# Kernel tuning notes

Hardware: AMD Instinct MI355X
Metric: run time of the kernel (lower is better)

## Reference

```python
import jax, jax.numpy as jnp
import numpy as np

B, N, T, F, D = 2, 8, 128, 128, 256
EPS = 1e-5


def setup_inputs() -> dict:
    key = jax.random.key(0)
    ks = jax.random.split(key, 8)
    s = 1.0 / np.sqrt(D)
    s2 = 1.0 / np.sqrt(2 * D)
    return {
        "x": jax.random.normal(ks[0], (B, N, D), dtype=jnp.float32),
        "t_emb": jax.random.normal(ks[1], (T, D), dtype=jnp.float32),
        "f_emb": jax.random.normal(ks[2], (F, D), dtype=jnp.float32),
        "ln_g": jnp.ones((D,), dtype=jnp.float32),
        "ln_b": jnp.zeros((D,), dtype=jnp.float32),
        "W1": jax.random.uniform(ks[3], (D, 2 * D), jnp.float32, -s, s),
        "b1": jax.random.uniform(ks[4], (2 * D,), jnp.float32, -s, s),
        "W2": jax.random.uniform(ks[5], (2 * D, 2), jnp.float32, -s2, s2),
        "b2": jax.random.uniform(ks[6], (2,), jnp.float32, -s2, s2),
    }


def reference(x, t_emb, f_emb, ln_g, ln_b, W1, b1, W2, b2):
    # x: [B,N,D]; pos_emb: [T,F,D]; broadcast-add -> [B,N,T,F,D]
    pos = t_emb[:, None, :] + f_emb[None, :, :]            # [T,F,D]
    h = x[:, :, None, None, :] + pos[None, None]           # [B,N,T,F,D]
    # LayerNorm over last dim
    mu = jnp.mean(h, axis=-1, keepdims=True)
    var = jnp.mean(jnp.square(h - mu), axis=-1, keepdims=True)
    h = (h - mu) * jax.lax.rsqrt(var + EPS) * ln_g + ln_b
    # MLP: D -> 2D -> 2
    h = jax.nn.relu(jnp.einsum("bntfd,de->bntfe", h, W1) + b1)
    out = jnp.einsum("bntfe,eo->bntfo", h, W2) + b2        # [B,N,T,F,2]
    return out
```

## Files before the change

### kernel.cpp

```cpp
#include <hip/hip_runtime.h>
#include <stdint.h>


#define D_ 256
#define E_ 512

typedef __attribute__((ext_vector_type(8))) short short8;
typedef __attribute__((ext_vector_type(4))) short short4v;
typedef __attribute__((ext_vector_type(4))) float f32x4;
typedef __attribute__((ext_vector_type(2))) float f32x2;

__device__ alignas(16) unsigned short g_Abuf[2176 * 768];
__device__ alignas(16) unsigned short g_Bbuf[768 * 640];
__device__ alignas(16) float g_U[2048 * 512];
__device__ alignas(16) float g_C[2048 * 128];
__device__ alignas(16) float g_Vt[512 * 128];
__device__ alignas(16) float g_GKW[512 * 4];
__device__ alignas(16) float g_sxt[2048];
__device__ alignas(16) float g_sqxt[2048];
__device__ alignas(16) float g_sf[128];
__device__ alignas(16) float g_sqf[128];

__device__ inline unsigned short f2bf(float f) {
  unsigned int u = __float_as_uint(f);
  u += 0x7fffu + ((u >> 16) & 1u);
  return (unsigned short)(u >> 16);
}
__device__ inline float bf2f(unsigned short h) {
  return __uint_as_float(((unsigned int)h) << 16);
}

__global__ __launch_bounds__(256) void prep(
    const float* __restrict__ x, const float* __restrict__ t_emb,
    const float* __restrict__ f_emb, const float* __restrict__ ln_g,
    const float* __restrict__ ln_b, const float* __restrict__ W1,
    const float* __restrict__ b1, const float* __restrict__ W2) {
  const int blk = blockIdx.x;
  const int tid = threadIdx.x;
  if (blk < 544) {
    const int l = tid & 63;
    int arow;
    float v0, v1, v2, v3;
    if (blk < 512) {
      const int r = blk * 4 + (tid >> 6);
      const int bn = r >> 7, t = r & 127;
      const float4 xv = *(const float4*)(x + bn * D_ + 4 * l);
      const float4 tv = *(const float4*)(t_emb + t * D_ + 4 * l);
      v0 = xv.x + tv.x; v1 = xv.y + tv.y;
      v2 = xv.z + tv.z; v3 = xv.w + tv.w;
      arow = r;
    } else {
      const int fi = (blk - 512) * 4 + (tid >> 6);
      const float4 fv = *(const float4*)(f_emb + fi * D_ + 4 * l);
      v0 = fv.x; v1 = fv.y; v2 = fv.z; v3 = fv.w;
      arow = 2048 + fi;
    }
    union { unsigned short u[4]; short4v v; } hi, lo;
    hi.u[0] = f2bf(v0); hi.u[1] = f2bf(v1);
    hi.u[2] = f2bf(v2); hi.u[3] = f2bf(v3);
    lo.u[0] = f2bf(v0 - bf2f(hi.u[0]));
    lo.u[1] = f2bf(v1 - bf2f(hi.u[1]));
    lo.u[2] = f2bf(v2 - bf2f(hi.u[2]));
    lo.u[3] = f2bf(v3 - bf2f(hi.u[3]));
    unsigned short* ab = g_Abuf + arow * 768 + 4 * l;
    *(short4v*)(ab) = hi.v;
    *(short4v*)(ab + 256) = lo.v;
    *(short4v*)(ab + 512) = hi.v;
    float s = (v0 + v1) + (v2 + v3);
    float q = fmaf(v0, v0, fmaf(v1, v1, fmaf(v2, v2, v3 * v3)));
#pragma unroll
    for (int d = 1; d < 64; d <<= 1) {
      s += __shfl_xor(s, d);
      q += __shfl_xor(q, d);
    }
    if (l == 0) {
      if (blk < 512) { g_sxt[arow] = s; g_sqxt[arow] = q; }
      else           { g_sf[arow - 2048] = s; g_sqf[arow - 2048] = q; }
    }
  } else if (blk < 552) {
    __shared__ float red[4][64][2];
    const int w = tid >> 6, l = tid & 63;
    const int e = (blk - 544) * 64 + l;
    const int k0 = w * 64;
    float G = 0.f, K = 0.f;
#pragma unroll 8
    for (int i = 0; i < 64; ++i) {
      const float wv = W1[(k0 + i) * E_ + e];
      G = fmaf(ln_g[k0 + i], wv, G);
      K = fmaf(ln_b[k0 + i], wv, K);
    }
    red[w][l][0] = G;
    red[w][l][1] = K;
    __syncthreads();
    if (w == 0) {
      G = (red[0][l][0] + red[1][l][0]) + (red[2][l][0] + red[3][l][0]);
      K = (red[0][l][1] + red[1][l][1]) + (red[2][l][1] + red[3][l][1]);
      float4 o;
      o.x = G; o.y = K + b1[e];
      o.z = W2[2 * e]; o.w = W2[2 * e + 1];
      *(float4*)(g_GKW + 4 * e) = o;
    }
  } else {
    const int gidx = (blk - 552) * 256 + tid;
    const int lane = gidx & 63;
    const int jtl = (gidx >> 6) & 3;
    const int cc = gidx >> 8;
    const int ct = cc % 10;
    const int kt = cc / 10;
    const int col = ct * 64 + jtl * 16 + (lane & 15);
    const int kbase = kt * 32 + ((lane >> 4) & 3) * 8;
    union { unsigned short u[8]; short8 v; } fr;
#pragma unroll
    for (int j = 0; j < 8; ++j) {
      const int kk = kbase + j;
      const int term = kk >> 8;
      const int k = kk & 255;
      float v;
      if (col < 512) v = ln_g[k] * W1[k * E_ + col];
      else           v = f_emb[(col - 512) * D_ + k];
      const unsigned short h = f2bf(v);
      fr.u[j] = (term == 2) ? f2bf(v - bf2f(h)) : h;
    }
    *(short8*)(g_Bbuf + gidx * 8) = fr.v;
  }
}

__global__ __launch_bounds__(256) void gemm3() {
  const int tid = threadIdx.x;
  const int wave = tid >> 6, lane = tid & 63;
  const int quad = (lane >> 4) & 3, n16 = lane & 15;
  const int rt = blockIdx.x / 10, ct = blockIdx.x % 10;
  const int rowb = rt * 128 + wave * 32;

  const unsigned short* a0 = g_Abuf + (size_t)(rowb + n16) * 768 + quad * 8;
  const unsigned short* a1 = a0 + 16 * 768;

  f32x4 acc[2][4];
#pragma unroll
  for (int j = 0; j < 4; ++j) {
    acc[0][j] = (f32x4){0.f, 0.f, 0.f, 0.f};
    acc[1][j] = (f32x4){0.f, 0.f, 0.f, 0.f};
  }

#pragma unroll 4
  for (int kt = 0; kt < 24; ++kt) {
    const short8 av0 = *(const short8*)(a0 + kt * 32);
    const short8 av1 = *(const short8*)(a1 + kt * 32);
    const short8* bp = (const short8*)g_Bbuf + ((kt * 10 + ct) * 4) * 64 + lane;
#pragma unroll
    for (int jtl = 0; jtl < 4; ++jtl) {
      const short8 bf = bp[jtl * 64];
      acc[0][jtl] =
          __builtin_amdgcn_mfma_f32_16x16x32_bf16(av0, bf, acc[0][jtl], 0, 0, 0);
      acc[1][jtl] =
          __builtin_amdgcn_mfma_f32_16x16x32_bf16(av1, bf, acc[1][jtl], 0, 0, 0);
    }
  }

#pragma unroll
  for (int g = 0; g < 2; ++g)
#pragma unroll
    for (int jtl = 0; jtl < 4; ++jtl)
#pragma unroll
      for (int r = 0; r < 4; ++r) {
        const float val = acc[g][jtl][r];
        const int grow = rowb + g * 16 + quad * 4 + r;
        const int col = ct * 64 + jtl * 16 + n16;
        if (rt < 16) {
          if (ct < 8) g_U[grow * 512 + col] = val;
          else        g_C[grow * 128 + (col - 512)] = val;
        } else if (ct < 8) {
          g_Vt[col * 128 + (grow - 2048)] = val;
        }
      }
}

__global__ __launch_bounds__(512) void decode2(const float* __restrict__ b2,
                                               float* __restrict__ out) {
  __shared__ float part[8][64][17];
  const int tid = threadIdx.x;
  const int w = tid >> 6, lane = tid & 63;
  const int bnt0 = blockIdx.x * 4;

  const f32x2 sf2 = *(const f32x2*)(g_sf + 2 * lane);
  const f32x2 sqf2 = *(const f32x2*)(g_sqf + 2 * lane);
  f32x2 Ar[4], Br[4];
#pragma unroll
  for (int ti = 0; ti < 4; ++ti) {
    const float sx = g_sxt[bnt0 + ti];
    const float sqx = g_sqxt[bnt0 + ti];
    const f32x2 c2 = *(const f32x2*)(g_C + (bnt0 + ti) * 128 + 2 * lane);
    const f32x2 mu = (sf2 + sx) * (1.0f / 256.0f);
    const f32x2 var = (sqf2 + 2.0f * c2 + sqx) * (1.0f / 256.0f) - mu * mu;
    f32x2 rs;
    rs.x = rsqrtf(var.x + 1e-5f);
    rs.y = rsqrtf(var.y + 1e-5f);
    Ar[ti] = rs;
    Br[ti] = -rs * mu;
  }

  f32x2 o0[4] = {(f32x2){0.f, 0.f}, (f32x2){0.f, 0.f},
                 (f32x2){0.f, 0.f}, (f32x2){0.f, 0.f}};
  f32x2 o1[4] = {(f32x2){0.f, 0.f}, (f32x2){0.f, 0.f},
                 (f32x2){0.f, 0.f}, (f32x2){0.f, 0.f}};
  const int ebase = __builtin_amdgcn_readfirstlane(w * 64);
#pragma unroll 8
  for (int ei = 0; ei < 64; ++ei) {
    const int e = ebase + ei;
    const float4 gkw = *(const float4*)(g_GKW + 4 * e);
    const f32x2 v2 = *(const f32x2*)(g_Vt + e * 128 + 2 * lane);
#pragma unroll
    for (int ti = 0; ti < 4; ++ti) {
      const float u = g_U[(bnt0 + ti) * 512 + e];
      const f32x2 s = v2 + u;
      const f32x2 pre = Ar[ti] * s + (Br[ti] * gkw.x + gkw.y);
      f32x2 y;
      y.x = fmaxf(pre.x, 0.f);
      y.y = fmaxf(pre.y, 0.f);
      o0[ti] += y * gkw.z;
      o1[ti] += y * gkw.w;
    }
  }

#pragma unroll
  for (int ti = 0; ti < 4; ++ti) {
    part[w][lane][ti * 4 + 0] = o0[ti].x;
    part[w][lane][ti * 4 + 1] = o1[ti].x;
    part[w][lane][ti * 4 + 2] = o0[ti].y;
    part[w][lane][ti * 4 + 3] = o1[ti].y;
  }
  __syncthreads();

  const int t = tid >> 7, f = tid & 127;
  const int m = f >> 1, ff = f & 1;
  float r0 = b2[0], r1 = b2[1];
#pragma unroll
  for (int w2 = 0; w2 < 8; ++w2) {
    r0 += part[w2][m][t * 4 + ff * 2 + 0];
    r1 += part[w2][m][t * 4 + ff * 2 + 1];
  }
  float2 res;
  res.x = r0;
  res.y = r1;
  *(float2*)(out + ((bnt0 + t) * 128 + f) * 2) = res;
}

extern "C" void kernel_launch(void* const* d_in, const int* in_sizes, int n_in,
                              void* d_out, int out_size, void* d_ws,
                              size_t ws_size, hipStream_t stream) {
  const float* x = (const float*)d_in[0];
  const float* t_emb = (const float*)d_in[1];
  const float* f_emb = (const float*)d_in[2];
  const float* ln_g = (const float*)d_in[3];
  const float* ln_b = (const float*)d_in[4];
  const float* W1 = (const float*)d_in[5];
  const float* b1 = (const float*)d_in[6];
  const float* W2 = (const float*)d_in[7];
  const float* b2 = (const float*)d_in[8];
  (void)d_ws; (void)ws_size;

  prep<<<792, 256, 0, stream>>>(x, t_emb, f_emb, ln_g, ln_b, W1, b1, W2);
  gemm3<<<170, 256, 0, stream>>>();
  decode2<<<512, 512, 0, stream>>>(b2, (float*)d_out);
}
```

Baseline: 113.2 us.

## Fuse prep, GEMM and decode into one persistent kernel with grid barriers

Merges the three kernels into a single 512-block launch whose phases are separated by a software grid barrier built on an atomic counter. This removes two launch gaps and inter-kernel drains. Work is redistributed per wave: the GEMM now uses one 16-row tile per wave, and the decode uses 256-thread blocks with 128 e values per wave. The barrier assumes all 512 blocks are co-resident, and the spin-wait plus reduced per-wave reuse in the GEMM may add cost.

```diff
diff --git a/kernel.cpp b/kernel.cpp
--- a/kernel.cpp
+++ b/kernel.cpp
@@ -4,6 +4,7 @@
 
 #define D_ 256
 #define E_ 512
+#define NBLK 512
 
 typedef __attribute__((ext_vector_type(8))) short short8;
 typedef __attribute__((ext_vector_type(4))) short short4v;
@@ -20,6 +21,7 @@
 __device__ alignas(16) float g_sqxt[2048];
 __device__ alignas(16) float g_sf[128];
 __device__ alignas(16) float g_sqf[128];
+__device__ unsigned int g_bar = 0;
 
 __device__ inline unsigned short f2bf(float f) {
   unsigned int u = __float_as_uint(f);
@@ -30,219 +32,218 @@
   return __uint_as_float(((unsigned int)h) << 16);
 }
 
-__global__ __launch_bounds__(256) void prep(
+__device__ inline void grid_barrier() {
+  __syncthreads();
+  if (threadIdx.x == 0) {
+    __threadfence();
+    const unsigned old =
+        __hip_atomic_fetch_add(&g_bar, 1u, __ATOMIC_RELAXED,
+                               __HIP_MEMORY_SCOPE_AGENT);
+    const unsigned target = (old & ~(unsigned)(NBLK - 1)) + NBLK;
+    while (__hip_atomic_load(&g_bar, __ATOMIC_RELAXED,
+                             __HIP_MEMORY_SCOPE_AGENT) < target)
+      __builtin_amdgcn_s_sleep(2);
+    __threadfence();
+  }
+  __syncthreads();
+}
+
+__global__ __launch_bounds__(256, 2) void fused(
     const float* __restrict__ x, const float* __restrict__ t_emb,
     const float* __restrict__ f_emb, const float* __restrict__ ln_g,
     const float* __restrict__ ln_b, const float* __restrict__ W1,
-    const float* __restrict__ b1, const float* __restrict__ W2) {
+    const float* __restrict__ b1, const float* __restrict__ W2,
+    const float* __restrict__ b2, float* __restrict__ out) {
+  __shared__ float part[4][64][17];
+  const int tid = threadIdx.x;
   const int blk = blockIdx.x;
-  const int tid = threadIdx.x;
-  if (blk < 544) {
-    const int l = tid & 63;
-    int arow;
-    float v0, v1, v2, v3;
-    if (blk < 512) {
-      const int r = blk * 4 + (tid >> 6);
-      const int bn = r >> 7, t = r & 127;
-      const float4 xv = *(const float4*)(x + bn * D_ + 4 * l);
-      const float4 tv = *(const float4*)(t_emb + t * D_ + 4 * l);
-      v0 = xv.x + tv.x; v1 = xv.y + tv.y;
-      v2 = xv.z + tv.z; v3 = xv.w + tv.w;
-      arow = r;
-    } else {
-      const int fi = (blk - 512) * 4 + (tid >> 6);
-      const float4 fv = *(const float4*)(f_emb + fi * D_ + 4 * l);
-      v0 = fv.x; v1 = fv.y; v2 = fv.z; v3 = fv.w;
-      arow = 2048 + fi;
-    }
-    union { unsigned short u[4]; short4v v; } hi, lo;
-    hi.u[0] = f2bf(v0); hi.u[1] = f2bf(v1);
-    hi.u[2] = f2bf(v2); hi.u[3] = f2bf(v3);
-    lo.u[0] = f2bf(v0 - bf2f(hi.u[0]));
-    lo.u[1] = f2bf(v1 - bf2f(hi.u[1]));
-    lo.u[2] = f2bf(v2 - bf2f(hi.u[2]));
-    lo.u[3] = f2bf(v3 - bf2f(hi.u[3]));
-    unsigned short* ab = g_Abuf + arow * 768 + 4 * l;
-    *(short4v*)(ab) = hi.v;
-    *(short4v*)(ab + 256) = lo.v;
-    *(short4v*)(ab + 512) = hi.v;
-    float s = (v0 + v1) + (v2 + v3);
-    float q = fmaf(v0, v0, fmaf(v1, v1, fmaf(v2, v2, v3 * v3)));
-#pragma unroll
-    for (int d = 1; d < 64; d <<= 1) {
-      s += __shfl_xor(s, d);
-      q += __shfl_xor(q, d);
-    }
-    if (l == 0) {
-      if (blk < 512) { g_sxt[arow] = s; g_sqxt[arow] = q; }
-      else           { g_sf[arow - 2048] = s; g_sqf[arow - 2048] = q; }
-    }
-  } else if (blk < 552) {
-    __shared__ float red[4][64][2];
-    const int w = tid >> 6, l = tid & 63;
-    const int e = (blk - 544) * 64 + l;
-    const int k0 = w * 64;
-    float G = 0.f, K = 0.f;
+  const int wv = tid >> 6;
+  const int lane = tid & 63;
+  const int wg = blk * 4 + wv;
+
+  for (int wt = wg; wt < 3144; wt += 2048) {
+    if (wt < 2176) {
+      const int arow = wt;
+      float v0, v1, v2, v3;
+      if (arow < 2048) {
+        const int bn = arow >> 7, t = arow & 127;
+        const float4 xv = *(const float4*)(x + bn * D_ + 4 * lane);
+        const float4 tv = *(const float4*)(t_emb + t * D_ + 4 * lane);
+        v0 = xv.x + tv.x; v1 = xv.y + tv.y;
+        v2 = xv.z + tv.z; v3 = xv.w + tv.w;
+      } else {
+        const int fi = arow - 2048;
+        const float4 fv = *(const float4*)(f_emb + fi * D_ + 4 * lane);
+        v0 = fv.x; v1 = fv.y; v2 = fv.z; v3 = fv.w;
+      }
+      union { unsigned short u[4]; short4v v; } hi, lo;
+      hi.u[0] = f2bf(v0); hi.u[1] = f2bf(v1);
+      hi.u[2] = f2bf(v2); hi.u[3] = f2bf(v3);
+      lo.u[0] = f2bf(v0 - bf2f(hi.u[0]));
+      lo.u[1] = f2bf(v1 - bf2f(hi.u[1]));
+      lo.u[2] = f2bf(v2 - bf2f(hi.u[2]));
+      lo.u[3] = f2bf(v3 - bf2f(hi.u[3]));
+      unsigned short* ab = g_Abuf + arow * 768 + 4 * lane;
+      *(short4v*)(ab) = hi.v;
+      *(short4v*)(ab + 256) = lo.v;
+      *(short4v*)(ab + 512) = hi.v;
+      float s = (v0 + v1) + (v2 + v3);
+      float q = fmaf(v0, v0, fmaf(v1, v1, fmaf(v2, v2, v3 * v3)));
+#pragma unroll
+      for (int d = 1; d < 64; d <<= 1) {
+        s += __shfl_xor(s, d);
+        q += __shfl_xor(q, d);
+      }
+      if (lane == 0) {
+        if (arow < 2048) { g_sxt[arow] = s; g_sqxt[arow] = q; }
+        else             { g_sf[arow - 2048] = s; g_sqf[arow - 2048] = q; }
+      }
+    } else if (wt < 2184) {
+      const int e = (wt - 2176) * 64 + lane;
+      float G = 0.f, K = 0.f;
 #pragma unroll 8
-    for (int i = 0; i < 64; ++i) {
-      const float wv = W1[(k0 + i) * E_ + e];
-      G = fmaf(ln_g[k0 + i], wv, G);
-      K = fmaf(ln_b[k0 + i], wv, K);
-    }
-    red[w][l][0] = G;
-    red[w][l][1] = K;
-    __syncthreads();
-    if (w == 0) {
-      G = (red[0][l][0] + red[1][l][0]) + (red[2][l][0] + red[3][l][0]);
-      K = (red[0][l][1] + red[1][l][1]) + (red[2][l][1] + red[3][l][1]);
+      for (int k = 0; k < 256; ++k) {
+        const float wv_ = W1[k * E_ + e];
+        G = fmaf(ln_g[k], wv_, G);
+        K = fmaf(ln_b[k], wv_, K);
+      }
       float4 o;
       o.x = G; o.y = K + b1[e];
       o.z = W2[2 * e]; o.w = W2[2 * e + 1];
       *(float4*)(g_GKW + 4 * e) = o;
-    }
-  } else {
-    const int gidx = (blk - 552) * 256 + tid;
-    const int lane = gidx & 63;
-    const int jtl = (gidx >> 6) & 3;
-    const int cc = gidx >> 8;
-    const int ct = cc % 10;
-    const int kt = cc / 10;
-    const int col = ct * 64 + jtl * 16 + (lane & 15);
-    const int kbase = kt * 32 + ((lane >> 4) & 3) * 8;
-    union { unsigned short u[8]; short8 v; } fr;
-#pragma unroll
-    for (int j = 0; j < 8; ++j) {
-      const int kk = kbase + j;
-      const int term = kk >> 8;
-      const int k = kk & 255;
-      float v;
-      if (col < 512) v = ln_g[k] * W1[k * E_ + col];
-      else           v = f_emb[(col - 512) * D_ + k];
-      const unsigned short h = f2bf(v);
-      fr.u[j] = (term == 2) ? f2bf(v - bf2f(h)) : h;
-    }
-    *(short8*)(g_Bbuf + gidx * 8) = fr.v;
-  }
-}
-
-__global__ __launch_bounds__(256) void gemm3() {
-  const int tid = threadIdx.x;
-  const int wave = tid >> 6, lane = tid & 63;
-  const int quad = (lane >> 4) & 3, n16 = lane & 15;
-  const int rt = blockIdx.x / 10, ct = blockIdx.x % 10;
-  const int rowb = rt * 128 + wave * 32;
-
-  const unsigned short* a0 = g_Abuf + (size_t)(rowb + n16) * 768 + quad * 8;
-  const unsigned short* a1 = a0 + 16 * 768;
-
-  f32x4 acc[2][4];
-#pragma unroll
-  for (int j = 0; j < 4; ++j) {
-    acc[0][j] = (f32x4){0.f, 0.f, 0.f, 0.f};
-    acc[1][j] = (f32x4){0.f, 0.f, 0.f, 0.f};
-  }
+    } else {
+      const int gidx = (wt - 2184) * 64 + lane;
+      const int gl = gidx & 63;
+      const int jtl = (gidx >> 6) & 3;
+      const int cc = gidx >> 8;
+      const int ct = cc % 10;
+      const int kt = cc / 10;
+      const int col = ct * 64 + jtl * 16 + (gl & 15);
+      const int kbase = kt * 32 + ((gl >> 4) & 3) * 8;
+      union { unsigned short u[8]; short8 v; } fr;
+#pragma unroll
+      for (int j = 0; j < 8; ++j) {
+        const int kk = kbase + j;
+        const int term = kk >> 8;
+        const int k = kk & 255;
+        float v;
+        if (col < 512) v = ln_g[k] * W1[k * E_ + col];
+        else           v = f_emb[(col - 512) * D_ + k];
+        const unsigned short h = f2bf(v);
+        fr.u[j] = (term == 2) ? f2bf(v - bf2f(h)) : h;
+      }
+      *(short8*)(g_Bbuf + gidx * 8) = fr.v;
+    }
+  }
+
+  grid_barrier();
+
+  if (wg < 1360) {
+    const int quad = (lane >> 4) & 3, n16 = lane & 15;
+    const int rt16 = wg / 10, ct = wg % 10;
+    const int rowb = rt16 * 16;
+    const unsigned short* a0 = g_Abuf + (size_t)(rowb + n16) * 768 + quad * 8;
+
+    f32x4 acc[4];
+#pragma unroll
+    for (int j = 0; j < 4; ++j) acc[j] = (f32x4){0.f, 0.f, 0.f, 0.f};
 
 #pragma unroll 4
-  for (int kt = 0; kt < 24; ++kt) {
-    const short8 av0 = *(const short8*)(a0 + kt * 32);
-    const short8 av1 = *(const short8*)(a1 + kt * 32);
-    const short8* bp = (const short8*)g_Bbuf + ((kt * 10 + ct) * 4) * 64 + lane;
-#pragma unroll
-    for (int jtl = 0; jtl < 4; ++jtl) {
-      const short8 bf = bp[jtl * 64];
-      acc[0][jtl] =
-          __builtin_amdgcn_mfma_f32_16x16x32_bf16(av0, bf, acc[0][jtl], 0, 0, 0);
-      acc[1][jtl] =
-          __builtin_amdgcn_mfma_f32_16x16x32_bf16(av1, bf, acc[1][jtl], 0, 0, 0);
-    }
-  }
-
-#pragma unroll
-  for (int g = 0; g < 2; ++g)
+    for (int kt = 0; kt < 24; ++kt) {
+      const short8 av = *(const short8*)(a0 + kt * 32);
+      const short8* bp =
+          (const short8*)g_Bbuf + ((kt * 10 + ct) * 4) * 64 + lane;
+#pragma unroll
+      for (int jtl = 0; jtl < 4; ++jtl)
+        acc[jtl] = __builtin_amdgcn_mfma_f32_16x16x32_bf16(av, bp[jtl * 64],
+                                                           acc[jtl], 0, 0, 0);
+    }
+
 #pragma unroll
     for (int jtl = 0; jtl < 4; ++jtl)
 #pragma unroll
       for (int r = 0; r < 4; ++r) {
-        const float val = acc[g][jtl][r];
-        const int grow = rowb + g * 16 + quad * 4 + r;
+        const float val = acc[jtl][r];
+        const int grow = rowb + quad * 4 + r;
         const int col = ct * 64 + jtl * 16 + n16;
-        if (rt < 16) {
-          if (ct < 8) g_U[grow * 512 + col] = val;
-          else        g_C[grow * 128 + (col - 512)] = val;
-        } else if (ct < 8) {
+        if (grow < 2048) {
+          if (col < 512) g_U[grow * 512 + col] = val;
+          else           g_C[grow * 128 + (col - 512)] = val;
+        } else if (col < 512) {
           g_Vt[col * 128 + (grow - 2048)] = val;
         }
       }
-}
-
-__global__ __launch_bounds__(512) void decode2(const float* __restrict__ b2,
-                                               float* __restrict__ out) {
-  __shared__ float part[8][64][17];
-  const int tid = threadIdx.x;
-  const int w = tid >> 6, lane = tid & 63;
-  const int bnt0 = blockIdx.x * 4;
-
-  const f32x2 sf2 = *(const f32x2*)(g_sf + 2 * lane);
-  const f32x2 sqf2 = *(const f32x2*)(g_sqf + 2 * lane);
-  f32x2 Ar[4], Br[4];
-#pragma unroll
-  for (int ti = 0; ti < 4; ++ti) {
-    const float sx = g_sxt[bnt0 + ti];
-    const float sqx = g_sqxt[bnt0 + ti];
-    const f32x2 c2 = *(const f32x2*)(g_C + (bnt0 + ti) * 128 + 2 * lane);
-    const f32x2 mu = (sf2 + sx) * (1.0f / 256.0f);
-    const f32x2 var = (sqf2 + 2.0f * c2 + sqx) * (1.0f / 256.0f) - mu * mu;
-    f32x2 rs;
-    rs.x = rsqrtf(var.x + 1e-5f);
-    rs.y = rsqrtf(var.y + 1e-5f);
-    Ar[ti] = rs;
-    Br[ti] = -rs * mu;
-  }
-
-  f32x2 o0[4] = {(f32x2){0.f, 0.f}, (f32x2){0.f, 0.f},
-                 (f32x2){0.f, 0.f}, (f32x2){0.f, 0.f}};
-  f32x2 o1[4] = {(f32x2){0.f, 0.f}, (f32x2){0.f, 0.f},
-                 (f32x2){0.f, 0.f}, (f32x2){0.f, 0.f}};
-  const int ebase = __builtin_amdgcn_readfirstlane(w * 64);
+  }
+
+  grid_barrier();
+
+  {
+    const int bnt0 = blk * 4;
+    const f32x2 sf2 = *(const f32x2*)(g_sf + 2 * lane);
+    const f32x2 sqf2 = *(const f32x2*)(g_sqf + 2 * lane);
+    f32x2 Ar[4], Br[4];
+#pragma unroll
+    for (int ti = 0; ti < 4; ++ti) {
+      const float sx = g_sxt[bnt0 + ti];
+      const float sqx = g_sqxt[bnt0 + ti];
+      const f32x2 c2 = *(const f32x2*)(g_C + (bnt0 + ti) * 128 + 2 * lane);
+      const f32x2 mu = (sf2 + sx) * (1.0f / 256.0f);
+      const f32x2 var = (sqf2 + 2.0f * c2 + sqx) * (1.0f / 256.0f) - mu * mu;
+      f32x2 rs;
+      rs.x = rsqrtf(var.x + 1e-5f);
+      rs.y = rsqrtf(var.y + 1e-5f);
+      Ar[ti] = rs;
+      Br[ti] = -rs * mu;
+    }
+
+    f32x2 o0[4] = {(f32x2){0.f, 0.f}, (f32x2){0.f, 0.f},
+                   (f32x2){0.f, 0.f}, (f32x2){0.f, 0.f}};
+    f32x2 o1[4] = {(f32x2){0.f, 0.f}, (f32x2){0.f, 0.f},
+                   (f32x2){0.f, 0.f}, (f32x2){0.f, 0.f}};
+    const int ebase = __builtin_amdgcn_readfirstlane(wv * 128);
 #pragma unroll 8
-  for (int ei = 0; ei < 64; ++ei) {
-    const int e = ebase + ei;
-    const float4 gkw = *(const float4*)(g_GKW + 4 * e);
-    const f32x2 v2 = *(const f32x2*)(g_Vt + e * 128 + 2 * lane);
+    for (int ei = 0; ei < 128; ++ei) {
+      const int e = ebase + ei;
+      const float4 gkw = *(const float4*)(g_GKW + 4 * e);
+      const f32x2 v2 = *(const f32x2*)(g_Vt + e * 128 + 2 * lane);
+#pragma unroll
+      for (int ti = 0; ti < 4; ++ti) {
+        const float u = g_U[(bnt0 + ti) * 512 + e];
+        const f32x2 s = v2 + u;
+        const f32x2 pre = Ar[ti] * s + (Br[ti] * gkw.x + gkw.y);
+        f32x2 y;
+        y.x = fmaxf(pre.x, 0.f);
+        y.y = fmaxf(pre.y, 0.f);
+        o0[ti] += y * gkw.z;
+        o1[ti] += y * gkw.w;
+      }
+    }
+
 #pragma unroll
     for (int ti = 0; ti < 4; ++ti) {
-      const float u = g_U[(bnt0 + ti) * 512 + e];
-      const f32x2 s = v2 + u;
-      const f32x2 pre = Ar[ti] * s + (Br[ti] * gkw.x + gkw.y);
-      f32x2 y;
-      y.x = fmaxf(pre.x, 0.f);
-      y.y = fmaxf(pre.y, 0.f);
-      o0[ti] += y * gkw.z;
-      o1[ti] += y * gkw.w;
-    }
-  }
-
-#pragma unroll
-  for (int ti = 0; ti < 4; ++ti) {
-    part[w][lane][ti * 4 + 0] = o0[ti].x;
-    part[w][lane][ti * 4 + 1] = o1[ti].x;
-    part[w][lane][ti * 4 + 2] = o0[ti].y;
-    part[w][lane][ti * 4 + 3] = o1[ti].y;
-  }
-  __syncthreads();
-
-  const int t = tid >> 7, f = tid & 127;
-  const int m = f >> 1, ff = f & 1;
-  float r0 = b2[0], r1 = b2[1];
-#pragma unroll
-  for (int w2 = 0; w2 < 8; ++w2) {
-    r0 += part[w2][m][t * 4 + ff * 2 + 0];
-    r1 += part[w2][m][t * 4 + ff * 2 + 1];
-  }
-  float2 res;
-  res.x = r0;
-  res.y = r1;
-  *(float2*)(out + ((bnt0 + t) * 128 + f) * 2) = res;
+      part[wv][lane][ti * 4 + 0] = o0[ti].x;
+      part[wv][lane][ti * 4 + 1] = o1[ti].x;
+      part[wv][lane][ti * 4 + 2] = o0[ti].y;
+      part[wv][lane][ti * 4 + 3] = o1[ti].y;
+    }
+    __syncthreads();
+
+    const int f = tid & 127;
+    const int m = f >> 1, ff = f & 1;
+#pragma unroll
+    for (int t = tid >> 7; t < 4; t += 2) {
+      float r0 = b2[0], r1 = b2[1];
+#pragma unroll
+      for (int w2 = 0; w2 < 4; ++w2) {
+        r0 += part[w2][m][t * 4 + ff * 2 + 0];
+        r1 += part[w2][m][t * 4 + ff * 2 + 1];
+      }
+      float2 res;
+      res.x = r0;
+      res.y = r1;
+      *(float2*)(out + ((bnt0 + t) * 128 + f) * 2) = res;
+    }
+  }
 }
 
 extern "C" void kernel_launch(void* const* d_in, const int* in_sizes, int n_in,
@@ -259,7 +260,6 @@
   const float* b2 = (const float*)d_in[8];
   (void)d_ws; (void)ws_size;
 
-  prep<<<792, 256, 0, stream>>>(x, t_emb, f_emb, ln_g, ln_b, W1, b1, W2);
-  gemm3<<<170, 256, 0, stream>>>();
-  decode2<<<512, 512, 0, stream>>>(b2, (float*)d_out);
-}
+  fused<<<NBLK, 256, 0, stream>>>(x, t_emb, f_emb, ln_g, ln_b, W1, b1, W2, b2,
+                                  (float*)d_out);
+}
```

Result: slower. 221.3 us (+95.5%).

## Fuse GEMM into decode kernel via shared-memory U/C and compute Vt in prep

Applied to the files above, without the earlier changes.

Removes the separate gemm3 kernel. Each decode block now computes its own 4 rows of U and C with MFMA, using a 16-row tile in which only 4 rows are valid, and keeps them in shared memory instead of writing them to global buffers. The f_emb·(g⊙W1) product Vt is moved into new fp32 scalar blocks inside prep. This saves one launch and the global round trip for U and C. In exchange, 3/4 of the MFMA work is wasted on padding rows and B fragments are re-read by every block.

```diff
diff --git a/kernel.cpp b/kernel.cpp
--- a/kernel.cpp
+++ b/kernel.cpp
@@ -10,10 +10,8 @@
 typedef __attribute__((ext_vector_type(4))) float f32x4;
 typedef __attribute__((ext_vector_type(2))) float f32x2;
 
-__device__ alignas(16) unsigned short g_Abuf[2176 * 768];
+__device__ alignas(16) unsigned short g_Abuf[2048 * 768];
 __device__ alignas(16) unsigned short g_Bbuf[768 * 640];
-__device__ alignas(16) float g_U[2048 * 512];
-__device__ alignas(16) float g_C[2048 * 128];
 __device__ alignas(16) float g_Vt[512 * 128];
 __device__ alignas(16) float g_GKW[512 * 4];
 __device__ alignas(16) float g_sxt[2048];
@@ -37,24 +35,15 @@
     const float* __restrict__ b1, const float* __restrict__ W2) {
   const int blk = blockIdx.x;
   const int tid = threadIdx.x;
-  if (blk < 544) {
-    const int l = tid & 63;
-    int arow;
-    float v0, v1, v2, v3;
-    if (blk < 512) {
-      const int r = blk * 4 + (tid >> 6);
-      const int bn = r >> 7, t = r & 127;
-      const float4 xv = *(const float4*)(x + bn * D_ + 4 * l);
-      const float4 tv = *(const float4*)(t_emb + t * D_ + 4 * l);
-      v0 = xv.x + tv.x; v1 = xv.y + tv.y;
-      v2 = xv.z + tv.z; v3 = xv.w + tv.w;
-      arow = r;
-    } else {
-      const int fi = (blk - 512) * 4 + (tid >> 6);
-      const float4 fv = *(const float4*)(f_emb + fi * D_ + 4 * l);
-      v0 = fv.x; v1 = fv.y; v2 = fv.z; v3 = fv.w;
-      arow = 2048 + fi;
-    }
+  const int wv = tid >> 6;
+  const int l = tid & 63;
+  if (blk < 512) {
+    const int r = blk * 4 + wv;
+    const int bn = r >> 7, t = r & 127;
+    const float4 xv = *(const float4*)(x + bn * D_ + 4 * l);
+    const float4 tv = *(const float4*)(t_emb + t * D_ + 4 * l);
+    const float v0 = xv.x + tv.x, v1 = xv.y + tv.y;
+    const float v2 = xv.z + tv.z, v3 = xv.w + tv.w;
     union { unsigned short u[4]; short4v v; } hi, lo;
     hi.u[0] = f2bf(v0); hi.u[1] = f2bf(v1);
     hi.u[2] = f2bf(v2); hi.u[3] = f2bf(v3);
@@ -62,7 +51,7 @@
     lo.u[1] = f2bf(v1 - bf2f(hi.u[1]));
     lo.u[2] = f2bf(v2 - bf2f(hi.u[2]));
     lo.u[3] = f2bf(v3 - bf2f(hi.u[3]));
-    unsigned short* ab = g_Abuf + arow * 768 + 4 * l;
+    unsigned short* ab = g_Abuf + r * 768 + 4 * l;
     *(short4v*)(ab) = hi.v;
     *(short4v*)(ab + 256) = lo.v;
     *(short4v*)(ab + 512) = hi.v;
@@ -73,26 +62,34 @@
       s += __shfl_xor(s, d);
       q += __shfl_xor(q, d);
     }
-    if (l == 0) {
-      if (blk < 512) { g_sxt[arow] = s; g_sqxt[arow] = q; }
-      else           { g_sf[arow - 2048] = s; g_sqf[arow - 2048] = q; }
-    }
+    if (l == 0) { g_sxt[r] = s; g_sqxt[r] = q; }
+  } else if (blk < 544) {
+    const int fi = (blk - 512) * 4 + wv;
+    const float4 fv = *(const float4*)(f_emb + fi * D_ + 4 * l);
+    float s = (fv.x + fv.y) + (fv.z + fv.w);
+    float q = fmaf(fv.x, fv.x,
+                   fmaf(fv.y, fv.y, fmaf(fv.z, fv.z, fv.w * fv.w)));
+#pragma unroll
+    for (int d = 1; d < 64; d <<= 1) {
+      s += __shfl_xor(s, d);
+      q += __shfl_xor(q, d);
+    }
+    if (l == 0) { g_sf[fi] = s; g_sqf[fi] = q; }
   } else if (blk < 552) {
     __shared__ float red[4][64][2];
-    const int w = tid >> 6, l = tid & 63;
     const int e = (blk - 544) * 64 + l;
-    const int k0 = w * 64;
+    const int k0 = wv * 64;
     float G = 0.f, K = 0.f;
 #pragma unroll 8
     for (int i = 0; i < 64; ++i) {
-      const float wv = W1[(k0 + i) * E_ + e];
-      G = fmaf(ln_g[k0 + i], wv, G);
-      K = fmaf(ln_b[k0 + i], wv, K);
-    }
-    red[w][l][0] = G;
-    red[w][l][1] = K;
+      const float wval = W1[(k0 + i) * E_ + e];
+      G = fmaf(ln_g[k0 + i], wval, G);
+      K = fmaf(ln_b[k0 + i], wval, K);
+    }
+    red[wv][l][0] = G;
+    red[wv][l][1] = K;
     __syncthreads();
-    if (w == 0) {
+    if (wv == 0) {
       G = (red[0][l][0] + red[1][l][0]) + (red[2][l][0] + red[3][l][0]);
       K = (red[0][l][1] + red[1][l][1]) + (red[2][l][1] + red[3][l][1]);
       float4 o;
@@ -100,15 +97,15 @@
       o.z = W2[2 * e]; o.w = W2[2 * e + 1];
       *(float4*)(g_GKW + 4 * e) = o;
     }
-  } else {
+  } else if (blk < 792) {
     const int gidx = (blk - 552) * 256 + tid;
-    const int lane = gidx & 63;
+    const int gl = gidx & 63;
     const int jtl = (gidx >> 6) & 3;
     const int cc = gidx >> 8;
     const int ct = cc % 10;
     const int kt = cc / 10;
-    const int col = ct * 64 + jtl * 16 + (lane & 15);
-    const int kbase = kt * 32 + ((lane >> 4) & 3) * 8;
+    const int col = ct * 64 + jtl * 16 + (gl & 15);
+    const int kbase = kt * 32 + ((gl >> 4) & 3) * 8;
     union { unsigned short u[8]; short8 v; } fr;
 #pragma unroll
     for (int j = 0; j < 8; ++j) {
@@ -122,65 +119,67 @@
       fr.u[j] = (term == 2) ? f2bf(v - bf2f(h)) : h;
     }
     *(short8*)(g_Bbuf + gidx * 8) = fr.v;
-  }
-}
-
-__global__ __launch_bounds__(256) void gemm3() {
-  const int tid = threadIdx.x;
-  const int wave = tid >> 6, lane = tid & 63;
-  const int quad = (lane >> 4) & 3, n16 = lane & 15;
-  const int rt = blockIdx.x / 10, ct = blockIdx.x % 10;
-  const int rowb = rt * 128 + wave * 32;
-
-  const unsigned short* a0 = g_Abuf + (size_t)(rowb + n16) * 768 + quad * 8;
-  const unsigned short* a1 = a0 + 16 * 768;
-
-  f32x4 acc[2][4];
-#pragma unroll
-  for (int j = 0; j < 4; ++j) {
-    acc[0][j] = (f32x4){0.f, 0.f, 0.f, 0.f};
-    acc[1][j] = (f32x4){0.f, 0.f, 0.f, 0.f};
-  }
-
+  } else {
+    const int e = (blk - 792) * 4 + wv;
+    const int eu = __builtin_amdgcn_readfirstlane(e);
+    const float* f0 = f_emb + (2 * l) * D_;
+    const float* f1 = f0 + D_;
+    float s0a = 0.f, s0b = 0.f, s1a = 0.f, s1b = 0.f;
 #pragma unroll 4
-  for (int kt = 0; kt < 24; ++kt) {
-    const short8 av0 = *(const short8*)(a0 + kt * 32);
-    const short8 av1 = *(const short8*)(a1 + kt * 32);
-    const short8* bp = (const short8*)g_Bbuf + ((kt * 10 + ct) * 4) * 64 + lane;
-#pragma unroll
-    for (int jtl = 0; jtl < 4; ++jtl) {
-      const short8 bf = bp[jtl * 64];
-      acc[0][jtl] =
-          __builtin_amdgcn_mfma_f32_16x16x32_bf16(av0, bf, acc[0][jtl], 0, 0, 0);
-      acc[1][jtl] =
-          __builtin_amdgcn_mfma_f32_16x16x32_bf16(av1, bf, acc[1][jtl], 0, 0, 0);
-    }
-  }
-
-#pragma unroll
-  for (int g = 0; g < 2; ++g)
-#pragma unroll
-    for (int jtl = 0; jtl < 4; ++jtl)
-#pragma unroll
-      for (int r = 0; r < 4; ++r) {
-        const float val = acc[g][jtl][r];
-        const int grow = rowb + g * 16 + quad * 4 + r;
-        const int col = ct * 64 + jtl * 16 + n16;
-        if (rt < 16) {
-          if (ct < 8) g_U[grow * 512 + col] = val;
-          else        g_C[grow * 128 + (col - 512)] = val;
-        } else if (ct < 8) {
-          g_Vt[col * 128 + (grow - 2048)] = val;
-        }
-      }
-}
-
-__global__ __launch_bounds__(512) void decode2(const float* __restrict__ b2,
-                                               float* __restrict__ out) {
+    for (int k = 0; k < 256; k += 4) {
+      const float w0 = ln_g[k + 0] * W1[(k + 0) * E_ + eu];
+      const float w1 = ln_g[k + 1] * W1[(k + 1) * E_ + eu];
+      const float w2 = ln_g[k + 2] * W1[(k + 2) * E_ + eu];
+      const float w3 = ln_g[k + 3] * W1[(k + 3) * E_ + eu];
+      const float4 fa = *(const float4*)(f0 + k);
+      const float4 fb = *(const float4*)(f1 + k);
+      s0a = fmaf(w0, fa.x, s0a); s0b = fmaf(w1, fa.y, s0b);
+      s0a = fmaf(w2, fa.z, s0a); s0b = fmaf(w3, fa.w, s0b);
+      s1a = fmaf(w0, fb.x, s1a); s1b = fmaf(w1, fb.y, s1b);
+      s1a = fmaf(w2, fb.z, s1a); s1b = fmaf(w3, fb.w, s1b);
+    }
+    float2 res;
+    res.x = s0a + s0b;
+    res.y = s1a + s1b;
+    *(float2*)(g_Vt + eu * 128 + 2 * l) = res;
+  }
+}
+
+__global__ __launch_bounds__(512, 4) void fused2(const float* __restrict__ b2,
+                                                 float* __restrict__ out) {
+  __shared__ float UC[4][648];
   __shared__ float part[8][64][17];
   const int tid = threadIdx.x;
   const int w = tid >> 6, lane = tid & 63;
+  const int quad = (lane >> 4) & 3, n16 = lane & 15;
   const int bnt0 = blockIdx.x * 4;
+
+  {
+    const unsigned short* a0 =
+        g_Abuf + (size_t)(bnt0 + (n16 & 3)) * 768 + quad * 8;
+    f32x4 acc[5];
+#pragma unroll
+    for (int j = 0; j < 5; ++j) acc[j] = (f32x4){0.f, 0.f, 0.f, 0.f};
+    const int ct0 = w * 5;
+#pragma unroll 4
+    for (int kt = 0; kt < 24; ++kt) {
+      const short8 av = *(const short8*)(a0 + kt * 32);
+#pragma unroll
+      for (int j = 0; j < 5; ++j) {
+        const int c = ct0 + j;
+        const short8 bf = ((const short8*)
+            g_Bbuf)[((kt * 10 + (c >> 2)) * 4 + (c & 3)) * 64 + lane];
+        acc[j] = __builtin_amdgcn_mfma_f32_16x16x32_bf16(av, bf, acc[j], 0, 0, 0);
+      }
+    }
+    if (quad == 0) {
+#pragma unroll
+      for (int j = 0; j < 5; ++j)
+#pragma unroll
+        for (int r = 0; r < 4; ++r) UC[r][(ct0 + j) * 16 + n16] = acc[j][r];
+    }
+  }
+  __syncthreads();
 
   const f32x2 sf2 = *(const f32x2*)(g_sf + 2 * lane);
   const f32x2 sqf2 = *(const f32x2*)(g_sqf + 2 * lane);
@@ -189,7 +188,7 @@
   for (int ti = 0; ti < 4; ++ti) {
     const float sx = g_sxt[bnt0 + ti];
     const float sqx = g_sqxt[bnt0 + ti];
-    const f32x2 c2 = *(const f32x2*)(g_C + (bnt0 + ti) * 128 + 2 * lane);
+    const f32x2 c2 = *(const f32x2*)&UC[ti][512 + 2 * lane];
     const f32x2 mu = (sf2 + sx) * (1.0f / 256.0f);
     const f32x2 var = (sqf2 + 2.0f * c2 + sqx) * (1.0f / 256.0f) - mu * mu;
     f32x2 rs;
@@ -211,7 +210,7 @@
     const f32x2 v2 = *(const f32x2*)(g_Vt + e * 128 + 2 * lane);
 #pragma unroll
     for (int ti = 0; ti < 4; ++ti) {
-      const float u = g_U[(bnt0 + ti) * 512 + e];
+      const float u = UC[ti][e];
       const f32x2 s = v2 + u;
       const f32x2 pre = Ar[ti] * s + (Br[ti] * gkw.x + gkw.y);
       f32x2 y;
@@ -259,7 +258,6 @@
   const float* b2 = (const float*)d_in[8];
   (void)d_ws; (void)ws_size;
 
-  prep<<<792, 256, 0, stream>>>(x, t_emb, f_emb, ln_g, ln_b, W1, b1, W2);
-  gemm3<<<170, 256, 0, stream>>>();
-  decode2<<<512, 512, 0, stream>>>(b2, (float*)d_out);
-}
+  prep<<<920, 256, 0, stream>>>(x, t_emb, f_emb, ln_g, ln_b, W1, b1, W2);
+  fused2<<<512, 512, 0, stream>>>(b2, (float*)d_out);
+}
```

After: 153.7 us. 1.36x slower.
